# Optimization experiments

Hardware: AMD Instinct MI355X
Metric: run time of the kernel (lower is better)

Reference implementation:

```python
import jax, jax.numpy as jnp
import numpy as np

SIG_DEPTH = 4  # matches sig_depth init arg


def _outer(a, b):
    # flattened tensor product: [B, m] x [B, n] -> [B, m*n] (row-major, matches signatory layout)
    return (a[:, :, None] * b[:, None, :]).reshape(a.shape[0], -1)


def setup_inputs() -> dict:
    key = jax.random.key(0)
    k1, k2 = jax.random.split(key)
    B, L, Cin = 64, 256, 7
    out_dim = 512
    C = Cin + 1
    sig_channels = sum(C ** k for k in range(1, SIG_DEPTH + 1))  # 4680
    inp = jax.random.normal(k1, (B, L, Cin), dtype=jnp.float32)
    W = jax.random.normal(k2, (out_dim, sig_channels), dtype=jnp.float32) * 0.02
    b = jnp.zeros((out_dim,), dtype=jnp.float32)
    return {"inp": inp, "W": W, "b": b}


def reference(inp, W, b):
    B, L, Cin = inp.shape
    # Augment: prepend time channel linspace(0, 1, L), keep original channels
    t = jnp.broadcast_to(jnp.linspace(0.0, 1.0, L, dtype=inp.dtype)[None, :, None], (B, L, 1))
    x = jnp.concatenate([t, inp], axis=-1)  # [B, L, C]
    C = Cin + 1
    d = SIG_DEPTH
    dx = jnp.transpose(x[:, 1:] - x[:, :-1], (1, 0, 2))  # [L-1, B, C] increments
    init = tuple(jnp.zeros((B, C ** (k + 1)), x.dtype) for k in range(d))  # identity signature (all zero levels)

    def step(levels, v):
        # exp(v) in the truncated tensor algebra: e_k = v^{(x)k} / k!
        e = [v]
        for k in range(1, d):
            e.append(_outer(e[-1], v) / (k + 1))
        # Chen's identity: new_k = a_k + e_k + sum_{i=1}^{k-1} a_i (x) e_{k-i}
        new = []
        for k in range(d):
            acc = levels[k] + e[k]
            for i in range(k):
                acc = acc + _outer(levels[i], e[k - 1 - i])
            new.append(acc)
        sig = jnp.concatenate(new, axis=-1)  # [B, sig_channels]
        return tuple(new), sig

    _, sigs = jax.lax.scan(step, init, dx)  # [L-1, B, sig_channels] (stream=True)
    sigs = jnp.transpose(sigs, (1, 0, 2))   # [B, L-1, sig_channels]
    return sigs @ W.T + b                   # [B, L-1, out_dim]
```

## Files before the change

### kernel.cpp

```cpp
#include <hip/hip_runtime.h>
#include <hip/hip_bf16.h>

#define BATCH 64
#define LSEQ 256
#define CIN 7
#define CC 8
#define NSIG 4680
#define KPAD 4736
#define TSTEPS 255
#define ODIM 512
#define NCHUNK 16
#define CH 16
#define NKT 74
#define BM 256
#define BN 128

typedef __attribute__((ext_vector_type(8))) unsigned short ushort8;
typedef __attribute__((ext_vector_type(8))) __bf16 bf16x8;
typedef __attribute__((ext_vector_type(4))) float f32x4;

__device__ __forceinline__ unsigned short f2bf(float x) {
    __hip_bfloat16 h = __float2bfloat16(x);
    return *(unsigned short*)&h;
}

#define GLDS16(gp, lp)                                                      \
    __builtin_amdgcn_global_load_lds(                                       \
        (const __attribute__((address_space(1))) void*)(gp),                \
        (__attribute__((address_space(3))) void*)(lp), 16, 0, 0)

__global__ __launch_bounds__(512) void sig_ckpt_kernel(const float* __restrict__ inp,
                                                       float* __restrict__ ckpt) {
    __shared__ float sDx[TSTEPS * CC];

    const int b   = blockIdx.x;
    const int tid = threadIdx.x;

    const float* ip = inp + (size_t)b * LSEQ * CIN;
    for (int i = tid; i < TSTEPS * CC; i += 512) {
        int t = i >> 3, c = i & 7;
        sDx[i] = (c == 0) ? (1.0f / 255.0f)
                          : ip[(t + 1) * CIN + (c - 1)] - ip[t * CIN + (c - 1)];
    }
    __syncthreads();

    const int i1 = tid >> 6;
    const int i2 = (tid >> 3) & 7;
    const int i3 = tid & 7;

    float a1own = 0.0f, a2own = 0.0f, a3 = 0.0f;
    float a4[8];
#pragma unroll
    for (int e = 0; e < 8; ++e) a4[e] = 0.0f;

    for (int t = 0; t < 240; ++t) {
        const float* v = &sDx[t * CC];
        const float4 vlo = *(const float4*)&v[0];
        const float4 vhi = *(const float4*)&v[4];
        const float va = v[i1], vb = v[i2], vc = v[i3];
        const float e3s = va * vb * vc * (1.0f / 6.0f);
        const float T4 = e3s * 0.25f + a1own * vb * vc * (1.0f / 6.0f)
                       + a2own * vc * 0.5f + a3;
        a4[0] += vlo.x * T4; a4[1] += vlo.y * T4;
        a4[2] += vlo.z * T4; a4[3] += vlo.w * T4;
        a4[4] += vhi.x * T4; a4[5] += vhi.y * T4;
        a4[6] += vhi.z * T4; a4[7] += vhi.w * T4;
        a3 += e3s + (a1own * vb * 0.5f + a2own) * vc;
        a2own += vb * (0.5f * va + a1own);
        a1own += va;

        if (((t + 1) & 15) == 0) {
            const int c = ((t + 1) >> 4) - 1;
            float* cp = ckpt + ((size_t)b * 15 + c) * NSIG;
            if ((tid & 63) == 0) cp[i1] = a1own;
            if ((tid & 7) == 0) cp[8 + (tid >> 3)] = a2own;
            cp[72 + tid] = a3;
            float4 q0 = {a4[0], a4[1], a4[2], a4[3]};
            float4 q1 = {a4[4], a4[5], a4[6], a4[7]};
            *(float4*)&cp[584 + tid * 8]     = q0;
            *(float4*)&cp[584 + tid * 8 + 4] = q1;
        }
    }
}

__global__ __launch_bounds__(512) void sig_write_kernel(const float* __restrict__ inp,
                                                        const float* __restrict__ ckpt,
                                                        unsigned short* __restrict__ sig) {
    __shared__ float sDx[CH * CC];

    const int chunk = blockIdx.x;
    const int b     = blockIdx.y;
    const int tid   = threadIdx.x;
    const int t0    = chunk * CH;
    const int t1    = (chunk == NCHUNK - 1) ? TSTEPS : t0 + CH;

    const float* ip = inp + (size_t)b * LSEQ * CIN;
    for (int i = tid; i < (t1 - t0) * CC; i += 512) {
        int t = t0 + (i >> 3), c = i & 7;
        sDx[i] = (c == 0) ? (1.0f / 255.0f)
                          : ip[(t + 1) * CIN + (c - 1)] - ip[t * CIN + (c - 1)];
    }
    __syncthreads();

    const int i1 = tid >> 6;
    const int i2 = (tid >> 3) & 7;
    const int i3 = tid & 7;

    float a1own, a2own, a3;
    float a4[8];
    if (chunk == 0) {
        a1own = a2own = a3 = 0.0f;
#pragma unroll
        for (int e = 0; e < 8; ++e) a4[e] = 0.0f;
    } else {
        const float* cp = ckpt + ((size_t)b * 15 + (chunk - 1)) * NSIG;
        a1own = cp[i1];
        a2own = cp[8 + (tid >> 3)];
        a3    = cp[72 + tid];
        float4 q0 = *(const float4*)&cp[584 + tid * 8];
        float4 q1 = *(const float4*)&cp[584 + tid * 8 + 4];
        a4[0] = q0.x; a4[1] = q0.y; a4[2] = q0.z; a4[3] = q0.w;
        a4[4] = q1.x; a4[5] = q1.y; a4[6] = q1.z; a4[7] = q1.w;
    }

    for (int t = t0; t < t1; ++t) {
        const float* v = &sDx[(t - t0) * CC];
        const float4 vlo = *(const float4*)&v[0];
        const float4 vhi = *(const float4*)&v[4];
        const float va = v[i1], vb = v[i2], vc = v[i3];
        const float e3s = va * vb * vc * (1.0f / 6.0f);
        const float T4 = e3s * 0.25f + a1own * vb * vc * (1.0f / 6.0f)
                       + a2own * vc * 0.5f + a3;
        a4[0] += vlo.x * T4; a4[1] += vlo.y * T4;
        a4[2] += vlo.z * T4; a4[3] += vlo.w * T4;
        a4[4] += vhi.x * T4; a4[5] += vhi.y * T4;
        a4[6] += vhi.z * T4; a4[7] += vhi.w * T4;
        a3 += e3s + (a1own * vb * 0.5f + a2own) * vc;
        a2own += vb * (0.5f * va + a1own);
        a1own += va;

        unsigned short* row = sig + ((size_t)b * TSTEPS + t) * KPAD;
        ushort8 pack;
#pragma unroll
        for (int e = 0; e < 8; ++e) pack[e] = f2bf(a4[e]);
        *(ushort8*)(row + 584 + tid * 8) = pack;
        row[72 + tid] = f2bf(a3);
        if ((tid & 63) == 0) row[i1] = f2bf(a1own);
        if ((tid & 7) == 0) row[8 + (tid >> 3)] = f2bf(a2own);
        if (tid >= 448 && tid < 504) row[4232 + tid] = 0;
    }
}

__global__ __launch_bounds__(256) void wcvt_kernel(const float* __restrict__ W,
                                                   unsigned short* __restrict__ Wb) {
    int idx = blockIdx.x * 256 + threadIdx.x;
    if (idx >= ODIM * KPAD) return;
    int n = idx / KPAD, k = idx - n * KPAD;
    Wb[idx] = (k < NSIG) ? f2bf(W[(size_t)n * NSIG + k]) : (unsigned short)0;
}

__global__ __launch_bounds__(512) void gemm_kernel(const unsigned short* __restrict__ A,
                                                   const unsigned short* __restrict__ Wb,
                                                   const float* __restrict__ bias,
                                                   float* __restrict__ out,
                                                   int Mrows) {
    __shared__ unsigned short As[3][BM * 64];
    __shared__ unsigned short Bs[3][BN * 64];

    const int tid = threadIdx.x;
    int nt, mt;
    if (gridDim.y == 64) {
        const int li = blockIdx.y * 4 + blockIdx.x;
        const int x  = li & 7;
        const int j  = li >> 3;
        mt = x * 8 + (j >> 2);
        nt = j & 3;
    } else {
        nt = blockIdx.x; mt = blockIdx.y;
    }
    const int lane = tid & 63;
    const int wv   = tid >> 6;
    const int wr   = wv >> 1;
    const int wc   = wv & 1;
    const int lr   = lane & 15;
    const int lk   = (lane >> 4) * 8;
    const int sb   = lr & 7;

    const f32x4 z4 = {0.0f, 0.0f, 0.0f, 0.0f};
    f32x4 acc[4][4];
#pragma unroll
    for (int i = 0; i < 4; ++i)
#pragma unroll
        for (int j = 0; j < 4; ++j) acc[i][j] = z4;

    const int srow = tid >> 3;
    const int gcb  = (tid & 7) ^ (srow & 7);
    const int scol = gcb * 8;

    const unsigned short* aptr[4];
    const unsigned short* bptr[2];
#pragma unroll
    for (int i = 0; i < 4; ++i) {
        int gr = mt * BM + i * 64 + srow;
        if (gr >= Mrows) gr = 0;
        aptr[i] = A + (size_t)gr * KPAD + scol;
    }
#pragma unroll
    for (int i = 0; i < 2; ++i)
        bptr[i] = Wb + (size_t)(nt * BN + i * 64 + srow) * KPAD + scol;

#define STAGE(buf, koff)                                                    \
    do {                                                                    \
        _Pragma("unroll")                                                   \
        for (int i_ = 0; i_ < 4; ++i_)                                      \
            GLDS16(aptr[i_] + (koff),                                       \
                   ((char*)As[buf]) + i_ * 8192 + tid * 16);                \
        _Pragma("unroll")                                                   \
        for (int i_ = 0; i_ < 2; ++i_)                                      \
            GLDS16(bptr[i_] + (koff),                                       \
                   ((char*)Bs[buf]) + i_ * 8192 + tid * 16);                \
    } while (0)

    STAGE(0, 0);
    STAGE(1, 64);
    asm volatile("s_waitcnt vmcnt(6)" ::: "memory");
    __builtin_amdgcn_sched_barrier(0);
    __builtin_amdgcn_s_barrier();
    __builtin_amdgcn_sched_barrier(0);

    int cur = 0, nxt = 1, nn = 2;
    for (int t = 0; t < NKT; ++t) {
        if (t + 2 < NKT) STAGE(nn, (t + 2) * 64);

        const unsigned short* as = &As[0][0] + cur * (BM * 64);
        const unsigned short* bs = &Bs[0][0] + cur * (BN * 64);
#pragma unroll
        for (int ks = 0; ks < 2; ++ks) {
            const int kb  = (ks * 32 + lk) >> 3;
            const int kel = (kb ^ sb) * 8;
            bf16x8 af[4], bf[4];
#pragma unroll
            for (int i = 0; i < 4; ++i)
                af[i] = *(const bf16x8*)&as[(wr * 64 + i * 16 + lr) * 64 + kel];
#pragma unroll
            for (int j = 0; j < 4; ++j)
                bf[j] = *(const bf16x8*)&bs[(wc * 64 + j * 16 + lr) * 64 + kel];
#pragma unroll
            for (int i = 0; i < 4; ++i)
#pragma unroll
                for (int j = 0; j < 4; ++j)
                    acc[i][j] = __builtin_amdgcn_mfma_f32_16x16x32_bf16(
                        af[i], bf[j], acc[i][j], 0, 0, 0);
        }

        if (t + 2 < NKT) {
            asm volatile("s_waitcnt vmcnt(6)" ::: "memory");
            __builtin_amdgcn_sched_barrier(0);
            __builtin_amdgcn_s_barrier();
            __builtin_amdgcn_sched_barrier(0);
        } else if (t + 1 < NKT) {
            asm volatile("s_waitcnt vmcnt(0)" ::: "memory");
            __builtin_amdgcn_sched_barrier(0);
            __builtin_amdgcn_s_barrier();
            __builtin_amdgcn_sched_barrier(0);
        }
        const int tmp = cur; cur = nxt; nxt = nn; nn = tmp;
    }

    float bn[4];
#pragma unroll
    for (int j = 0; j < 4; ++j)
        bn[j] = bias[nt * BN + wc * 64 + j * 16 + lr];

#pragma unroll
    for (int i = 0; i < 4; ++i) {
        const int mbase = mt * BM + wr * 64 + i * 16 + (lane >> 4) * 4;
#pragma unroll
        for (int r = 0; r < 4; ++r) {
            const int m = mbase + r;
            if (m < Mrows) {
#pragma unroll
                for (int j = 0; j < 4; ++j) {
                    const int n = nt * BN + wc * 64 + j * 16 + lr;
                    out[(size_t)m * ODIM + n] = acc[i][j][r] + bn[j];
                }
            }
        }
    }
#undef STAGE
}

extern "C" void kernel_launch(void* const* d_in, const int* in_sizes, int n_in,
                              void* d_out, int out_size, void* d_ws, size_t ws_size,
                              hipStream_t stream) {
    const float* inp  = (const float*)d_in[0];
    const float* W    = (const float*)d_in[1];
    const float* bias = (const float*)d_in[2];
    float* out = (float*)d_out;

    const size_t wbBytes = (size_t)ODIM * KPAD * sizeof(unsigned short);
    const size_t sigPB   = (size_t)TSTEPS * KPAD * sizeof(unsigned short);
    const size_t ckptPB  = (size_t)15 * NSIG * sizeof(float);
    const size_t perB    = sigPB + ckptPB;

    int nbMax = (int)((ws_size - wbBytes) / perB);
    if (nbMax > BATCH) nbMax = BATCH;
    if (nbMax < 1) nbMax = 1;

    unsigned short* sig  = (unsigned short*)d_ws;
    float*          ckpt = (float*)((char*)d_ws + (size_t)nbMax * sigPB);
    unsigned short* Wb   = (unsigned short*)((char*)d_ws + (ws_size - wbBytes));

    wcvt_kernel<<<(ODIM * KPAD + 255) / 256, 256, 0, stream>>>(W, Wb);

    for (int b0 = 0; b0 < BATCH; b0 += nbMax) {
        const int nb = (b0 + nbMax <= BATCH) ? nbMax : (BATCH - b0);
        const int Mrows = nb * TSTEPS;
        const float* ipb = inp + (size_t)b0 * LSEQ * CIN;
        sig_ckpt_kernel<<<nb, 512, 0, stream>>>(ipb, ckpt);
        sig_write_kernel<<<dim3(NCHUNK, nb), 512, 0, stream>>>(ipb, ckpt, sig);
        gemm_kernel<<<dim3(ODIM / BN, (Mrows + BM - 1) / BM), 512, 0, stream>>>(
            sig, Wb, bias, out + (size_t)b0 * TSTEPS * ODIM, Mrows);
    }
}
```

Measured before the change: 176.8 us.

## Interleave global-to-LDS prefetch with MFMA phases and raise wave priority

Splits each K-tile iteration of the GEMM into two half-steps. Each half issues a subset of the global-to-LDS loads for the tile after next, interleaved between LDS fragment reads and the MFMA cluster, with extra barriers around each MFMA burst. MFMA sections are wrapped in s_setprio(1) so waves in the compute phase get issue priority. The aim is to spread memory issue and overlap it with matrix work, at the cost of more workgroup barriers per iteration.

```diff
diff --git a/kernel.cpp b/kernel.cpp
--- a/kernel.cpp
+++ b/kernel.cpp
@@ -183,7 +183,7 @@
     const int wr   = wv >> 1;
     const int wc   = wv & 1;
     const int lr   = lane & 15;
-    const int lk   = (lane >> 4) * 8;
+    const int lq   = lane >> 4;
     const int sb   = lr & 7;
 
     const f32x4 z4 = {0.0f, 0.0f, 0.0f, 0.0f};
@@ -209,7 +209,10 @@
     for (int i = 0; i < 2; ++i)
         bptr[i] = Wb + (size_t)(nt * BN + i * 64 + srow) * KPAD + scol;
 
-#define STAGE(buf, koff)                                                    \
+    const int kel0 = ((lq)     ^ sb) * 8;
+    const int kel1 = ((4 + lq) ^ sb) * 8;
+
+#define STAGE_ALL(buf, koff)                                                \
     do {                                                                    \
         _Pragma("unroll")                                                   \
         for (int i_ = 0; i_ < 4; ++i_)                                      \
@@ -221,8 +224,8 @@
                    ((char*)Bs[buf]) + i_ * 8192 + tid * 16);                \
     } while (0)
 
-    STAGE(0, 0);
-    STAGE(1, 64);
+    STAGE_ALL(0, 0);
+    STAGE_ALL(1, 64);
     asm volatile("s_waitcnt vmcnt(6)" ::: "memory");
     __builtin_amdgcn_sched_barrier(0);
     __builtin_amdgcn_s_barrier();
@@ -230,40 +233,77 @@
 
     int cur = 0, nxt = 1, nn = 2;
     for (int t = 0; t < NKT; ++t) {
-        if (t + 2 < NKT) STAGE(nn, (t + 2) * 64);
-
         const unsigned short* as = &As[0][0] + cur * (BM * 64);
         const unsigned short* bs = &Bs[0][0] + cur * (BN * 64);
-#pragma unroll
-        for (int ks = 0; ks < 2; ++ks) {
-            const int kb  = (ks * 32 + lk) >> 3;
-            const int kel = (kb ^ sb) * 8;
+        const bool st = (t + 2 < NKT);
+        const int koff = (t + 2) * 64;
+        char* dstA = (char*)As[0] + nn * (BM * 64 * 2);
+        char* dstB = (char*)Bs[0] + nn * (BN * 64 * 2);
+
+        {
             bf16x8 af[4], bf[4];
 #pragma unroll
             for (int i = 0; i < 4; ++i)
-                af[i] = *(const bf16x8*)&as[(wr * 64 + i * 16 + lr) * 64 + kel];
+                af[i] = *(const bf16x8*)&as[(wr * 64 + i * 16 + lr) * 64 + kel0];
 #pragma unroll
             for (int j = 0; j < 4; ++j)
-                bf[j] = *(const bf16x8*)&bs[(wc * 64 + j * 16 + lr) * 64 + kel];
+                bf[j] = *(const bf16x8*)&bs[(wc * 64 + j * 16 + lr) * 64 + kel0];
+            if (st) {
+                GLDS16(aptr[0] + koff, dstA + 0 * 8192 + tid * 16);
+                GLDS16(aptr[1] + koff, dstA + 1 * 8192 + tid * 16);
+                GLDS16(aptr[2] + koff, dstA + 2 * 8192 + tid * 16);
+            }
+            __builtin_amdgcn_sched_barrier(0);
+            __builtin_amdgcn_s_barrier();
+            asm volatile("s_waitcnt lgkmcnt(0)" ::: "memory");
+            __builtin_amdgcn_sched_barrier(0);
+            __builtin_amdgcn_s_setprio(1);
 #pragma unroll
             for (int i = 0; i < 4; ++i)
 #pragma unroll
                 for (int j = 0; j < 4; ++j)
                     acc[i][j] = __builtin_amdgcn_mfma_f32_16x16x32_bf16(
                         af[i], bf[j], acc[i][j], 0, 0, 0);
+            __builtin_amdgcn_s_setprio(0);
+            __builtin_amdgcn_sched_barrier(0);
+            __builtin_amdgcn_s_barrier();
         }
 
-        if (t + 2 < NKT) {
-            asm volatile("s_waitcnt vmcnt(6)" ::: "memory");
+        {
+            bf16x8 af[4], bf[4];
+#pragma unroll
+            for (int i = 0; i < 4; ++i)
+                af[i] = *(const bf16x8*)&as[(wr * 64 + i * 16 + lr) * 64 + kel1];
+#pragma unroll
+            for (int j = 0; j < 4; ++j)
+                bf[j] = *(const bf16x8*)&bs[(wc * 64 + j * 16 + lr) * 64 + kel1];
+            if (st) {
+                GLDS16(aptr[3] + koff, dstA + 3 * 8192 + tid * 16);
+                GLDS16(bptr[0] + koff, dstB + 0 * 8192 + tid * 16);
+                GLDS16(bptr[1] + koff, dstB + 1 * 8192 + tid * 16);
+            }
             __builtin_amdgcn_sched_barrier(0);
             __builtin_amdgcn_s_barrier();
-            __builtin_amdgcn_sched_barrier(0);
-        } else if (t + 1 < NKT) {
-            asm volatile("s_waitcnt vmcnt(0)" ::: "memory");
+            asm volatile("s_waitcnt lgkmcnt(0)" ::: "memory");
+            __builtin_amdgcn_sched_barrier(0);
+            __builtin_amdgcn_s_setprio(1);
+#pragma unroll
+            for (int i = 0; i < 4; ++i)
+#pragma unroll
+                for (int j = 0; j < 4; ++j)
+                    acc[i][j] = __builtin_amdgcn_mfma_f32_16x16x32_bf16(
+                        af[i], bf[j], acc[i][j], 0, 0, 0);
+            __builtin_amdgcn_s_setprio(0);
+            __builtin_amdgcn_sched_barrier(0);
+            if (st) {
+                asm volatile("s_waitcnt vmcnt(6)" ::: "memory");
+            } else if (t + 1 < NKT) {
+                asm volatile("s_waitcnt vmcnt(0)" ::: "memory");
+            }
             __builtin_amdgcn_sched_barrier(0);
             __builtin_amdgcn_s_barrier();
-            __builtin_amdgcn_sched_barrier(0);
         }
+
         const int tmp = cur; cur = nxt; nxt = nn; nn = tmp;
     }
 
@@ -274,7 +314,7 @@
 
 #pragma unroll
     for (int i = 0; i < 4; ++i) {
-        const int mbase = mt * BM + wr * 64 + i * 16 + (lane >> 4) * 4;
+        const int mbase = mt * BM + wr * 64 + i * 16 + lq * 4;
 #pragma unroll
         for (int r = 0; r < 4; ++r) {
             const int m = mbase + r;
@@ -287,7 +327,7 @@
             }
         }
     }
-#undef STAGE
+#undef STAGE_ALL
 }
 
 extern "C" void kernel_launch(void* const* d_in, const int* in_sizes, int n_in,
```

Result: faster. 153.1 us (-13.4%).
